# Performance work log

Measured on AMD Instinct MI355X. Metric: run time of the kernel, lower is better.

## Reference

```python
import jax, jax.numpy as jnp
import numpy as np

N, D = 16384, 64      # samples, state dimension (input_size)
H1, H2 = 256, 256     # hidden widths


def setup_inputs() -> dict:
    key = jax.random.key(0)
    ks = jax.random.split(key, 7)
    S = jax.random.normal(ks[0], (N, D), jnp.float32)
    Sdot = jax.random.normal(ks[1], (N, D), jnp.float32)
    W1 = jax.random.normal(ks[2], (H1, D), jnp.float32) / np.float32(np.sqrt(D))
    b1 = jax.random.normal(ks[3], (H1,), jnp.float32) * 0.1
    W2 = jax.random.normal(ks[4], (H2, H1), jnp.float32) / np.float32(np.sqrt(H1))
    b2 = jax.random.normal(ks[5], (H2,), jnp.float32) * 0.1
    W3 = jax.random.normal(ks[6], (1, H2), jnp.float32) / np.float32(np.sqrt(H2))
    return {"S": S, "Sdot": Sdot, "W1": W1, "b1": b1, "W2": W2, "b2": b2, "W3": W3}


def _forward_tensors(S, layers, W_last):
    # Manual MLP forward with per-sample Jacobian propagation.
    # SQUARE activation: act(z) = z^2, act'(z) = 2z.
    # torch's diag_embed(act_der) @ J is fused as elementwise row-scaling.
    n, d = S.shape
    y = S
    J = jnp.broadcast_to(jnp.eye(d, dtype=S.dtype), (n, d, d))  # [N, d, d]
    for W, b in layers:
        z = y @ W.T + b                      # [N, h]
        J = jnp.einsum('hp,npd->nhd', W, J)  # W @ J per sample
        J = (2.0 * z)[:, :, None] * J        # diag(2z) @ J as row scaling
        y = z * z                            # SQUARE activation
    nn_out = (y @ W_last.T)[:, 0]            # [N]
    grad_nn = jnp.einsum('h,nhd->nd', W_last[0], J)  # [N, d]
    return nn_out, grad_nn


def reference(S, Sdot, W1, b1, W2, b2, W3):
    nn_out, grad_nn = _forward_tensors(S, [(W1, b1), (W2, b2)], W3)
    circle = jnp.sum(S * S, axis=1)          # [N]
    F = circle
    dF = 2.0 * S
    V = nn_out * F
    gradV = nn_out[:, None] * dF + grad_nn * F[:, None]  # product rule
    Vdot = jnp.sum(gradV * Sdot, axis=1)
    return (V, Vdot, circle)
```

## Files before the change

### kernel.cpp

```cpp
#include <hip/hip_runtime.h>

typedef __attribute__((ext_vector_type(8))) short bf16x8;
typedef __attribute__((ext_vector_type(4))) short bf16x4;
typedef __attribute__((ext_vector_type(4))) float f32x4;

constexpr int N  = 16384;
constexpr int D  = 64;
constexpr int H  = 256;
constexpr int SB = 32;
constexpr int PITCH = 272;
constexpr int PLANE = 32 * PITCH;
constexpr int STAGE = 8 * PITCH;

__device__ __forceinline__ ushort f2bf(float x) {
    uint u = __float_as_uint(x);
    u += 0x7fffu + ((u >> 16) & 1u);
    return (ushort)(u >> 16);
}
__device__ __forceinline__ float bf2f(ushort h) {
    return __uint_as_float(((uint)h) << 16);
}
__device__ __forceinline__ int swz(int g, int i) {
    return i ^ ((i >> 2) & 3) ^ ((g & 1) << 1);
}

__global__ void prep_weights(const float* __restrict__ W1, const float* __restrict__ W2,
                             ushort* __restrict__ ws) {
    const int t = blockIdx.x * 256 + threadIdx.x;
    if (t < 8192) {
        const int h1g = t >> 8;
        const int h2  = t & 255;
        const float* src = W2 + h2 * 256 + h1g * 8;
        bf16x8 hi;
        #pragma unroll
        for (int j = 0; j < 8; ++j) hi[j] = (short)f2bf(src[j]);
        *reinterpret_cast<bf16x8*>(ws + 32768 + (h1g * 256 + h2) * 8) = hi;
    } else if (t < 10240) {
        const int u  = t - 8192;
        const int dg = u >> 8;
        const int h1 = u & 255;
        const float* src = W1 + h1 * 64 + dg * 8;
        bf16x8 hi, lo;
        #pragma unroll
        for (int j = 0; j < 8; ++j) {
            const float x = src[j];
            const ushort xh = f2bf(x);
            hi[j] = (short)xh;
            lo[j] = (short)f2bf(x - bf2f(xh));
        }
        const int d1 = (dg * 256 + h1) * 8;
        *reinterpret_cast<bf16x8*>(ws + d1)         = hi;
        *reinterpret_cast<bf16x8*>(ws + 16384 + d1) = lo;
    }
}

__global__ __launch_bounds__(256, 2) void fused_mfma(
    const float* __restrict__ S,  const float* __restrict__ Sdot,
    const float* __restrict__ b1v, const float* __restrict__ b2v,
    const float* __restrict__ W3, const ushort* __restrict__ ws,
    float* __restrict__ out)
{
    __shared__ ushort U[4 * STAGE + 2 * PLANE];
    __shared__ float  red[2][4][32];
    __shared__ float  csd[32][2];

    ushort* const sH = U;
    ushort* const sL = U + STAGE;
    ushort* const dH = U + 2 * STAGE;
    ushort* const dL = U + 3 * STAGE;
    ushort* const yH = U + 4 * STAGE;
    ushort* const pH = U + 4 * STAGE + PLANE;

    const int t   = threadIdx.x;
    const int l   = t & 63;
    const int wid = t >> 6;
    const int lg  = l >> 4;
    const int lc  = l & 15;
    const int s0  = blockIdx.x * SB;

    int hh[4];
    #pragma unroll
    for (int tt = 0; tt < 4; ++tt) hh[tt] = (wid * 4 + tt) * 16 + lc;

    bf16x8 B1h[2][4], B1l[2][4];
    #pragma unroll
    for (int kc = 0; kc < 2; ++kc) {
        const int g = kc * 4 + lg;
        #pragma unroll
        for (int tt = 0; tt < 4; ++tt) {
            const int o = (g * 256 + hh[tt]) * 8;
            B1h[kc][tt] = *reinterpret_cast<const bf16x8*>(ws + o);
            B1l[kc][tt] = *reinterpret_cast<const bf16x8*>(ws + 16384 + o);
        }
    }
    bf16x8 nbh[4];
    #pragma unroll
    for (int tt = 0; tt < 4; ++tt)
        nbh[tt] = *reinterpret_cast<const bf16x8*>(ws + 32768 + (lg * 256 + hh[tt]) * 8);

    float bb1[4], bb2[4], w3v[4];
    #pragma unroll
    for (int tt = 0; tt < 4; ++tt) {
        bb1[tt] = b1v[hh[tt]]; bb2[tt] = b2v[hh[tt]]; w3v[tt] = W3[hh[tt]];
    }

    {
        const int i    = t >> 3;
        const int g    = t & 7;
        const float* sp = S    + (size_t)(s0 + i) * D + g * 8;
        const float* dp = Sdot + (size_t)(s0 + i) * D + g * 8;
        const float4 s_a = reinterpret_cast<const float4*>(sp)[0];
        const float4 s_b = reinterpret_cast<const float4*>(sp)[1];
        const float4 d_a = reinterpret_cast<const float4*>(dp)[0];
        const float4 d_b = reinterpret_cast<const float4*>(dp)[1];
        const float sv[8] = {s_a.x,s_a.y,s_a.z,s_a.w,s_b.x,s_b.y,s_b.z,s_b.w};
        const float dv[8] = {d_a.x,d_a.y,d_a.z,d_a.w,d_b.x,d_b.y,d_b.z,d_b.w};
        bf16x8 vsh, vsl, vdh, vdl;
        float c = 0.f, sd = 0.f;
        #pragma unroll
        for (int j = 0; j < 8; ++j) {
            c  += sv[j] * sv[j];
            sd += sv[j] * dv[j];
            const ushort hs = f2bf(sv[j]);
            vsh[j] = (short)hs; vsl[j] = (short)f2bf(sv[j] - bf2f(hs));
            const ushort hd = f2bf(dv[j]);
            vdh[j] = (short)hd; vdl[j] = (short)f2bf(dv[j] - bf2f(hd));
        }
        const int off = g * PITCH + swz(g, i) * 8;
        *reinterpret_cast<bf16x8*>(&sH[off]) = vsh;
        *reinterpret_cast<bf16x8*>(&sL[off]) = vsl;
        *reinterpret_cast<bf16x8*>(&dH[off]) = vdh;
        *reinterpret_cast<bf16x8*>(&dL[off]) = vdl;
        #pragma unroll
        for (int o = 1; o < 8; o <<= 1) { c += __shfl_xor(c, o); sd += __shfl_xor(sd, o); }
        if ((t & 7) == 0) { csd[i][0] = c; csd[i][1] = sd; }
    }
    __syncthreads();

    bf16x8 ash[2][2], asl[2][2], adh[2][2], adl[2][2];
    #pragma unroll
    for (int kc = 0; kc < 2; ++kc) {
        const int g = kc * 4 + lg;
        #pragma unroll
        for (int mt = 0; mt < 2; ++mt) {
            const int off = g * PITCH + swz(g, mt * 16 + lc) * 8;
            ash[kc][mt] = *reinterpret_cast<const bf16x8*>(&sH[off]);
            asl[kc][mt] = *reinterpret_cast<const bf16x8*>(&sL[off]);
            adh[kc][mt] = *reinterpret_cast<const bf16x8*>(&dH[off]);
            adl[kc][mt] = *reinterpret_cast<const bf16x8*>(&dL[off]);
        }
    }
    f32x4 z1acc[2][4], u1acc[2][4];
    #pragma unroll
    for (int mt = 0; mt < 2; ++mt)
        #pragma unroll
        for (int tt = 0; tt < 4; ++tt) {
            z1acc[mt][tt] = (f32x4){0,0,0,0};
            u1acc[mt][tt] = (f32x4){0,0,0,0};
        }
    #pragma unroll
    for (int kc = 0; kc < 2; ++kc) {
        __builtin_amdgcn_s_setprio(1);
        #pragma unroll
        for (int tt = 0; tt < 4; ++tt) {
            #pragma unroll
            for (int mt = 0; mt < 2; ++mt) {
                z1acc[mt][tt] = __builtin_amdgcn_mfma_f32_16x16x32_bf16(ash[kc][mt], B1h[kc][tt], z1acc[mt][tt], 0,0,0);
                z1acc[mt][tt] = __builtin_amdgcn_mfma_f32_16x16x32_bf16(asl[kc][mt], B1h[kc][tt], z1acc[mt][tt], 0,0,0);
                z1acc[mt][tt] = __builtin_amdgcn_mfma_f32_16x16x32_bf16(ash[kc][mt], B1l[kc][tt], z1acc[mt][tt], 0,0,0);
                u1acc[mt][tt] = __builtin_amdgcn_mfma_f32_16x16x32_bf16(adh[kc][mt], B1h[kc][tt], u1acc[mt][tt], 0,0,0);
                u1acc[mt][tt] = __builtin_amdgcn_mfma_f32_16x16x32_bf16(adl[kc][mt], B1h[kc][tt], u1acc[mt][tt], 0,0,0);
                u1acc[mt][tt] = __builtin_amdgcn_mfma_f32_16x16x32_bf16(adh[kc][mt], B1l[kc][tt], u1acc[mt][tt], 0,0,0);
            }
        }
        __builtin_amdgcn_s_setprio(0);
    }

    #pragma unroll
    for (int tt = 0; tt < 4; ++tt) {
        const int grp = hh[tt] >> 3;
        const int jb  = grp * PITCH + (hh[tt] & 7);
        #pragma unroll
        for (int mt = 0; mt < 2; ++mt) {
            #pragma unroll
            for (int r = 0; r < 4; ++r) {
                const float z  = z1acc[mt][tt][r] + bb1[tt];
                const float pv = 2.f * z * u1acc[mt][tt][r];
                const int ii = swz(grp, mt * 16 + lg * 4 + r);
                yH[jb + ii * 8] = f2bf(z * z);
                pH[jb + ii * 8] = f2bf(pv);
            }
        }
    }
    __syncthreads();

    f32x4 z2acc[2][4], qacc[2][4];
    #pragma unroll
    for (int mt = 0; mt < 2; ++mt)
        #pragma unroll
        for (int tt = 0; tt < 4; ++tt) {
            z2acc[mt][tt] = (f32x4){0,0,0,0};
            qacc[mt][tt]  = (f32x4){0,0,0,0};
        }
    #pragma unroll
    for (int kc = 0; kc < 8; ++kc) {
        const int g = kc * 4 + lg;
        bf16x8 bh[4];
        #pragma unroll
        for (int tt = 0; tt < 4; ++tt) bh[tt] = nbh[tt];
        if (kc < 7) {
            const int gn = (kc + 1) * 4 + lg;
            #pragma unroll
            for (int tt = 0; tt < 4; ++tt)
                nbh[tt] = *reinterpret_cast<const bf16x8*>(ws + 32768 + (gn * 256 + hh[tt]) * 8);
        }
        bf16x8 ayh[2], aph[2];
        #pragma unroll
        for (int mt = 0; mt < 2; ++mt) {
            const int off = g * PITCH + swz(g, mt * 16 + lc) * 8;
            ayh[mt] = *reinterpret_cast<const bf16x8*>(&yH[off]);
            aph[mt] = *reinterpret_cast<const bf16x8*>(&pH[off]);
        }
        __builtin_amdgcn_s_setprio(1);
        #pragma unroll
        for (int tt = 0; tt < 4; ++tt) {
            #pragma unroll
            for (int mt = 0; mt < 2; ++mt) {
                z2acc[mt][tt] = __builtin_amdgcn_mfma_f32_16x16x32_bf16(ayh[mt], bh[tt], z2acc[mt][tt], 0,0,0);
                qacc[mt][tt]  = __builtin_amdgcn_mfma_f32_16x16x32_bf16(aph[mt], bh[tt], qacc[mt][tt], 0,0,0);
            }
        }
        __builtin_amdgcn_s_setprio(0);
    }

    float nnp[2][4], gdp[2][4];
    #pragma unroll
    for (int mt = 0; mt < 2; ++mt)
        #pragma unroll
        for (int r = 0; r < 4; ++r) { nnp[mt][r] = 0.f; gdp[mt][r] = 0.f; }
    #pragma unroll
    for (int tt = 0; tt < 4; ++tt) {
        #pragma unroll
        for (int mt = 0; mt < 2; ++mt) {
            #pragma unroll
            for (int r = 0; r < 4; ++r) {
                const float z = z2acc[mt][tt][r] + bb2[tt];
                nnp[mt][r] += w3v[tt] * z * z;
                gdp[mt][r] += 2.f * w3v[tt] * z * qacc[mt][tt][r];
            }
        }
    }
    #pragma unroll
    for (int mt = 0; mt < 2; ++mt)
        #pragma unroll
        for (int r = 0; r < 4; ++r) {
            float a = nnp[mt][r], b = gdp[mt][r];
            #pragma unroll
            for (int o = 1; o < 16; o <<= 1) { a += __shfl_xor(a, o); b += __shfl_xor(b, o); }
            if (lc == 0) {
                red[0][wid][mt * 16 + lg * 4 + r] = a;
                red[1][wid][mt * 16 + lg * 4 + r] = b;
            }
        }
    __syncthreads();

    if (t < SB) {
        const int i = t;
        float nn = 0.f, gd = 0.f;
        #pragma unroll
        for (int w = 0; w < 4; ++w) { nn += red[0][w][i]; gd += red[1][w][i]; }
        const float c  = csd[i][0];
        const float sd = csd[i][1];
        const int n = s0 + i;
        out[n]         = nn * c;
        out[N + n]     = 2.f * nn * sd + c * gd;
        out[2 * N + n] = c;
    }
}

extern "C" void kernel_launch(void* const* d_in, const int* in_sizes, int n_in,
                              void* d_out, int out_size, void* d_ws, size_t ws_size,
                              hipStream_t stream) {
    const float* S    = (const float*)d_in[0];
    const float* Sdot = (const float*)d_in[1];
    const float* W1   = (const float*)d_in[2];
    const float* b1   = (const float*)d_in[3];
    const float* W2   = (const float*)d_in[4];
    const float* b2   = (const float*)d_in[5];
    const float* W3   = (const float*)d_in[6];
    float* out = (float*)d_out;
    ushort* ws = (ushort*)d_ws;

    prep_weights<<<40, 256, 0, stream>>>(W1, W2, ws);
    fused_mfma<<<N / SB, 256, 0, stream>>>(S, Sdot, b1, b2, W3, ws, out);
}
```

Measured before the change: 20.42 us.

## Fuse weight bf16 conversion into main kernel and use packed cvt instructions

Drops the separate prep_weights launch, so the main kernel reads fp32 W1/W2 directly and converts them to bf16 hi/lo fragments in registers. Conversions now use the v_cvt_pk_bf16_f32 packed instruction instead of manual bit-twiddling rounding. This removes a kernel launch and its serialization, but doubles the bytes fetched for W2 per block and adds conversion ALU work inside the MFMA loop for every block.

After: 27.28 us. 1.34x slower.

```diff
diff --git a/kernel.cpp b/kernel.cpp
--- a/kernel.cpp
+++ b/kernel.cpp
@@ -1,7 +1,6 @@
 #include <hip/hip_runtime.h>
 
 typedef __attribute__((ext_vector_type(8))) short bf16x8;
-typedef __attribute__((ext_vector_type(4))) short bf16x4;
 typedef __attribute__((ext_vector_type(4))) float f32x4;
 
 constexpr int N  = 16384;
@@ -17,48 +16,41 @@
     u += 0x7fffu + ((u >> 16) & 1u);
     return (ushort)(u >> 16);
 }
-__device__ __forceinline__ float bf2f(ushort h) {
-    return __uint_as_float(((uint)h) << 16);
+__device__ __forceinline__ uint cvtpk(float e0, float e1) {
+    uint r;
+    asm("v_cvt_pk_bf16_f32 %0, %1, %2" : "=v"(r) : "v"(e0), "v"(e1));
+    return r;
+}
+union frag_u { bf16x8 v; uint u[4]; };
+
+__device__ __forceinline__ bf16x8 pack_hi(const float4& a, const float4& b) {
+    frag_u f;
+    f.u[0] = cvtpk(a.x, a.y); f.u[1] = cvtpk(a.z, a.w);
+    f.u[2] = cvtpk(b.x, b.y); f.u[3] = cvtpk(b.z, b.w);
+    return f.v;
+}
+__device__ __forceinline__ bf16x8 pack_lo(const float4& a, const float4& b, bf16x8 hi) {
+    frag_u h; h.v = hi;
+    frag_u f;
+    f.u[0] = cvtpk(a.x - __uint_as_float(h.u[0] << 16),
+                   a.y - __uint_as_float(h.u[0] & 0xffff0000u));
+    f.u[1] = cvtpk(a.z - __uint_as_float(h.u[1] << 16),
+                   a.w - __uint_as_float(h.u[1] & 0xffff0000u));
+    f.u[2] = cvtpk(b.x - __uint_as_float(h.u[2] << 16),
+                   b.y - __uint_as_float(h.u[2] & 0xffff0000u));
+    f.u[3] = cvtpk(b.z - __uint_as_float(h.u[3] << 16),
+                   b.w - __uint_as_float(h.u[3] & 0xffff0000u));
+    return f.v;
 }
 __device__ __forceinline__ int swz(int g, int i) {
     return i ^ ((i >> 2) & 3) ^ ((g & 1) << 1);
 }
 
-__global__ void prep_weights(const float* __restrict__ W1, const float* __restrict__ W2,
-                             ushort* __restrict__ ws) {
-    const int t = blockIdx.x * 256 + threadIdx.x;
-    if (t < 8192) {
-        const int h1g = t >> 8;
-        const int h2  = t & 255;
-        const float* src = W2 + h2 * 256 + h1g * 8;
-        bf16x8 hi;
-        #pragma unroll
-        for (int j = 0; j < 8; ++j) hi[j] = (short)f2bf(src[j]);
-        *reinterpret_cast<bf16x8*>(ws + 32768 + (h1g * 256 + h2) * 8) = hi;
-    } else if (t < 10240) {
-        const int u  = t - 8192;
-        const int dg = u >> 8;
-        const int h1 = u & 255;
-        const float* src = W1 + h1 * 64 + dg * 8;
-        bf16x8 hi, lo;
-        #pragma unroll
-        for (int j = 0; j < 8; ++j) {
-            const float x = src[j];
-            const ushort xh = f2bf(x);
-            hi[j] = (short)xh;
-            lo[j] = (short)f2bf(x - bf2f(xh));
-        }
-        const int d1 = (dg * 256 + h1) * 8;
-        *reinterpret_cast<bf16x8*>(ws + d1)         = hi;
-        *reinterpret_cast<bf16x8*>(ws + 16384 + d1) = lo;
-    }
-}
-
 __global__ __launch_bounds__(256, 2) void fused_mfma(
     const float* __restrict__ S,  const float* __restrict__ Sdot,
-    const float* __restrict__ b1v, const float* __restrict__ b2v,
-    const float* __restrict__ W3, const ushort* __restrict__ ws,
-    float* __restrict__ out)
+    const float* __restrict__ W1, const float* __restrict__ b1v,
+    const float* __restrict__ W2, const float* __restrict__ b2v,
+    const float* __restrict__ W3, float* __restrict__ out)
 {
     __shared__ ushort U[4 * STAGE + 2 * PLANE];
     __shared__ float  red[2][4][32];
@@ -88,15 +80,20 @@
         const int g = kc * 4 + lg;
         #pragma unroll
         for (int tt = 0; tt < 4; ++tt) {
-            const int o = (g * 256 + hh[tt]) * 8;
-            B1h[kc][tt] = *reinterpret_cast<const bf16x8*>(ws + o);
-            B1l[kc][tt] = *reinterpret_cast<const bf16x8*>(ws + 16384 + o);
-        }
-    }
-    bf16x8 nbh[4];
-    #pragma unroll
-    for (int tt = 0; tt < 4; ++tt)
-        nbh[tt] = *reinterpret_cast<const bf16x8*>(ws + 32768 + (lg * 256 + hh[tt]) * 8);
+            const float* wp = W1 + hh[tt] * D + g * 8;
+            const float4 a = *reinterpret_cast<const float4*>(wp);
+            const float4 b = *reinterpret_cast<const float4*>(wp + 4);
+            B1h[kc][tt] = pack_hi(a, b);
+            B1l[kc][tt] = pack_lo(a, b, B1h[kc][tt]);
+        }
+    }
+    float4 nf0[4], nf1[4];
+    #pragma unroll
+    for (int tt = 0; tt < 4; ++tt) {
+        const float* wp = W2 + hh[tt] * H + lg * 8;
+        nf0[tt] = *reinterpret_cast<const float4*>(wp);
+        nf1[tt] = *reinterpret_cast<const float4*>(wp + 4);
+    }
 
     float bb1[4], bb2[4], w3v[4];
     #pragma unroll
@@ -105,27 +102,22 @@
     }
 
     {
-        const int i    = t >> 3;
-        const int g    = t & 7;
+        const int i = t >> 3;
+        const int g = t & 7;
         const float* sp = S    + (size_t)(s0 + i) * D + g * 8;
         const float* dp = Sdot + (size_t)(s0 + i) * D + g * 8;
         const float4 s_a = reinterpret_cast<const float4*>(sp)[0];
         const float4 s_b = reinterpret_cast<const float4*>(sp)[1];
         const float4 d_a = reinterpret_cast<const float4*>(dp)[0];
         const float4 d_b = reinterpret_cast<const float4*>(dp)[1];
-        const float sv[8] = {s_a.x,s_a.y,s_a.z,s_a.w,s_b.x,s_b.y,s_b.z,s_b.w};
-        const float dv[8] = {d_a.x,d_a.y,d_a.z,d_a.w,d_b.x,d_b.y,d_b.z,d_b.w};
-        bf16x8 vsh, vsl, vdh, vdl;
-        float c = 0.f, sd = 0.f;
-        #pragma unroll
-        for (int j = 0; j < 8; ++j) {
-            c  += sv[j] * sv[j];
-            sd += sv[j] * dv[j];
-            const ushort hs = f2bf(sv[j]);
-            vsh[j] = (short)hs; vsl[j] = (short)f2bf(sv[j] - bf2f(hs));
-            const ushort hd = f2bf(dv[j]);
-            vdh[j] = (short)hd; vdl[j] = (short)f2bf(dv[j] - bf2f(hd));
-        }
+        const bf16x8 vsh = pack_hi(s_a, s_b);
+        const bf16x8 vsl = pack_lo(s_a, s_b, vsh);
+        const bf16x8 vdh = pack_hi(d_a, d_b);
+        const bf16x8 vdl = pack_lo(d_a, d_b, vdh);
+        float c  = s_a.x*s_a.x + s_a.y*s_a.y + s_a.z*s_a.z + s_a.w*s_a.w
+                 + s_b.x*s_b.x + s_b.y*s_b.y + s_b.z*s_b.z + s_b.w*s_b.w;
+        float sd = s_a.x*d_a.x + s_a.y*d_a.y + s_a.z*d_a.z + s_a.w*d_a.w
+                 + s_b.x*d_b.x + s_b.y*d_b.y + s_b.z*d_b.z + s_b.w*d_b.w;
         const int off = g * PITCH + swz(g, i) * 8;
         *reinterpret_cast<bf16x8*>(&sH[off]) = vsh;
         *reinterpret_cast<bf16x8*>(&sL[off]) = vsl;
@@ -207,12 +199,15 @@
         const int g = kc * 4 + lg;
         bf16x8 bh[4];
         #pragma unroll
-        for (int tt = 0; tt < 4; ++tt) bh[tt] = nbh[tt];
+        for (int tt = 0; tt < 4; ++tt) bh[tt] = pack_hi(nf0[tt], nf1[tt]);
         if (kc < 7) {
             const int gn = (kc + 1) * 4 + lg;
             #pragma unroll
-            for (int tt = 0; tt < 4; ++tt)
-                nbh[tt] = *reinterpret_cast<const bf16x8*>(ws + 32768 + (gn * 256 + hh[tt]) * 8);
+            for (int tt = 0; tt < 4; ++tt) {
+                const float* wp = W2 + hh[tt] * H + gn * 8;
+                nf0[tt] = *reinterpret_cast<const float4*>(wp);
+                nf1[tt] = *reinterpret_cast<const float4*>(wp + 4);
+            }
         }
         bf16x8 ayh[2], aph[2];
         #pragma unroll
@@ -289,8 +284,6 @@
     const float* b2   = (const float*)d_in[5];
     const float* W3   = (const float*)d_in[6];
     float* out = (float*)d_out;
-    ushort* ws = (ushort*)d_ws;
-
-    prep_weights<<<40, 256, 0, stream>>>(W1, W2, ws);
-    fused_mfma<<<N / SB, 256, 0, stream>>>(S, Sdot, b1, b2, W3, ws, out);
-}
+
+    fused_mfma<<<N / SB, 256, 0, stream>>>(S, Sdot, W1, b1, W2, b2, W3, out);
+}
```
